# Performance work log

Hardware: AMD Instinct MI355X
Metric: run time of the kernel (lower is better)

## Reference

```python
import jax, jax.numpy as jnp
import numpy as np

M = 262144      # total tokens
K = 64          # n_channels (input dim)
N = 64          # expert_size (output dim)
E = 8           # n_experts


def setup_inputs() -> dict:
    key = jax.random.key(0)
    k1, k2, k3 = jax.random.split(key, 3)
    x = jax.random.normal(k1, (M, K), dtype=jnp.float32)
    sel = jax.random.randint(k2, (M,), 0, E, dtype=jnp.int32)
    w = jax.random.normal(k3, (E, K, N), dtype=jnp.float32)
    return {"x": x, "sel": sel, "w": w}


def reference(x, sel, w):
    # cvmm: out[m] = x[m] @ w[sel[m]]  (per-token expert GEMM)
    # Loop over the small fixed expert set; accumulate masked dense GEMMs
    # instead of materializing w[sel] ([M,K,N], which would be huge).
    E_ = w.shape[0]
    out = jnp.zeros((x.shape[0], w.shape[2]), dtype=x.dtype)
    for e in range(E_):
        mask = (sel == e)[:, None]           # [M,1]
        out = out + jnp.where(mask, x @ w[e], jnp.zeros((), x.dtype))
    return out
```

## Files before the change

kernel.cpp:

```cpp
#include <hip/hip_runtime.h>


typedef __bf16 bf16x8 __attribute__((ext_vector_type(8)));
typedef float floatx4 __attribute__((ext_vector_type(4)));

#define MT 8

__global__ __launch_bounds__(256, 4) void cvmm_kernel(
    const float* __restrict__ x,
    const int* __restrict__ sel,
    const float* __restrict__ w,
    float* __restrict__ out,
    int M)
{
    const int lane = threadIdx.x & 63;
    const int wave = threadIdx.x >> 6;
    const int n0   = wave << 4;
    const int quad = lane >> 4;
    const int l16  = lane & 15;

    floatx4 bfp[8][2];
#pragma unroll
    for (int e = 0; e < 8; ++e) {
#pragma unroll
        for (int t = 0; t < 2; ++t) {
            const float* wp = w + ((e * 64 + t * 32 + quad * 8) * 64) + (n0 + l16);
            bf16x8 f;
#pragma unroll
            for (int j = 0; j < 8; ++j) {
                f[j] = (__bf16)wp[j * 64];
            }
            bfp[e][t] = __builtin_bit_cast(floatx4, f);
        }
    }
#pragma unroll
    for (int e = 0; e < 8; ++e) {
#pragma unroll
        for (int t = 0; t < 2; ++t) {
            asm volatile("" : "+v"(bfp[e][t]));
        }
    }

    bf16x8 zf;
#pragma unroll
    for (int j = 0; j < 8; ++j) zf[j] = (__bf16)0.0f;

    const int mt0 = blockIdx.x * MT;

    floatx4 pa0, pa1, pa2, pa3;
    int ps;
    {
        const int m0 = mt0 << 4;
        const float* xp = x + (size_t)(m0 + l16) * 64 + quad * 8;
        pa0 = *(const floatx4*)(xp);
        pa1 = *(const floatx4*)(xp + 4);
        pa2 = *(const floatx4*)(xp + 32);
        pa3 = *(const floatx4*)(xp + 36);
        ps  = sel[m0 + l16];
    }

#pragma unroll
    for (int i = 0; i < MT; ++i) {
        const floatx4 a0 = pa0, a1 = pa1, a2 = pa2, a3 = pa3;
        const int s = ps;

        if (i + 1 < MT) {
            const int m0n = (mt0 + i + 1) << 4;
            const float* xp = x + (size_t)(m0n + l16) * 64 + quad * 8;
            pa0 = *(const floatx4*)(xp);
            pa1 = *(const floatx4*)(xp + 4);
            pa2 = *(const floatx4*)(xp + 32);
            pa3 = *(const floatx4*)(xp + 36);
            ps  = sel[m0n + l16];
        }

        bf16x8 af0, af1;
#pragma unroll
        for (int j = 0; j < 4; ++j) {
            af0[j]     = (__bf16)a0[j];
            af0[j + 4] = (__bf16)a1[j];
            af1[j]     = (__bf16)a2[j];
            af1[j + 4] = (__bf16)a3[j];
        }

        floatx4 c0 = {0.0f, 0.0f, 0.0f, 0.0f};
        floatx4 c1 = {0.0f, 0.0f, 0.0f, 0.0f};
#pragma unroll
        for (int e = 0; e < 8; ++e) {
            const bool ok = (s == e);
            bf16x8 a0m = ok ? af0 : zf;
            bf16x8 a1m = ok ? af1 : zf;
            c0 = __builtin_amdgcn_mfma_f32_16x16x32_bf16(
                     a0m, __builtin_bit_cast(bf16x8, bfp[e][0]), c0, 0, 0, 0);
            c1 = __builtin_amdgcn_mfma_f32_16x16x32_bf16(
                     a1m, __builtin_bit_cast(bf16x8, bfp[e][1]), c1, 0, 0, 0);
        }

        const int m0 = (mt0 + i) << 4;
        float* op = out + (size_t)(m0 + quad * 4) * 64 + n0 + l16;
#pragma unroll
        for (int r = 0; r < 4; ++r) {
            op[(size_t)r * 64] = c0[r] + c1[r];
        }
    }
}

extern "C" void kernel_launch(void* const* d_in, const int* in_sizes, int n_in,
                              void* d_out, int out_size, void* d_ws, size_t ws_size,
                              hipStream_t stream) {
    const float* x   = (const float*)d_in[0];
    const int*   sel = (const int*)d_in[1];
    const float* w   = (const float*)d_in[2];
    float*       out = (float*)d_out;

    const int M = in_sizes[0] / 64;
    const int mtiles = M / 16;
    const int blocks = (mtiles + MT - 1) / MT;

    cvmm_kernel<<<blocks, 256, 0, stream>>>(x, sel, w, out, M);
}
```

Baseline: 145.7 us.

## Stage x tiles through swizzled double-buffered LDS, converting to bf16 once

Before this change, each of the four waves loaded and converted the full 16x64 x tile itself, so every block read and converted x four times. Now the block cooperatively loads 64-token chunks with coalesced float4 loads and converts them to bf16 once. It writes them into XOR-swizzled, double-buffered LDS that the waves read as MFMA A fragments. The next chunk is prefetched into registers while the current one computes. This costs LDS capacity and a __syncthreads per chunk, and the launch now assumes M is divisible by 256.

```diff
diff --git a/kernel.cpp b/kernel.cpp
--- a/kernel.cpp
+++ b/kernel.cpp
@@ -2,9 +2,11 @@
 
 
 typedef __bf16 bf16x8 __attribute__((ext_vector_type(8)));
-typedef float floatx4 __attribute__((ext_vector_type(4)));
+typedef __bf16 bf16x4 __attribute__((ext_vector_type(4)));
+typedef float  floatx4 __attribute__((ext_vector_type(4)));
 
-#define MT 8
+#define NCHUNK 4
+#define CHUNK_LDS 8192
 
 __global__ __launch_bounds__(256, 4) void cvmm_kernel(
     const float* __restrict__ x,
@@ -13,95 +15,111 @@
     float* __restrict__ out,
     int M)
 {
-    const int lane = threadIdx.x & 63;
-    const int wave = threadIdx.x >> 6;
-    const int n0   = wave << 4;
-    const int quad = lane >> 4;
+    __shared__ __align__(16) unsigned char lds[2 * CHUNK_LDS];
+
+    const int T    = threadIdx.x;
+    const int lane = T & 63;
+    const int wv   = T >> 6;
+    const int q    = lane >> 4;
     const int l16  = lane & 15;
+    const int n0   = wv << 4;
 
     floatx4 bfp[8][2];
 #pragma unroll
     for (int e = 0; e < 8; ++e) {
 #pragma unroll
         for (int t = 0; t < 2; ++t) {
-            const float* wp = w + ((e * 64 + t * 32 + quad * 8) * 64) + (n0 + l16);
+            const float* wp = w + ((e * 64 + t * 32 + q * 8) * 64) + (n0 + l16);
             bf16x8 f;
 #pragma unroll
-            for (int j = 0; j < 8; ++j) {
-                f[j] = (__bf16)wp[j * 64];
-            }
+            for (int j = 0; j < 8; ++j) f[j] = (__bf16)wp[j * 64];
             bfp[e][t] = __builtin_bit_cast(floatx4, f);
         }
     }
 #pragma unroll
-    for (int e = 0; e < 8; ++e) {
+    for (int e = 0; e < 8; ++e)
 #pragma unroll
-        for (int t = 0; t < 2; ++t) {
+        for (int t = 0; t < 2; ++t)
             asm volatile("" : "+v"(bfp[e][t]));
-        }
-    }
 
     bf16x8 zf;
 #pragma unroll
     for (int j = 0; j < 8; ++j) zf[j] = (__bf16)0.0f;
 
-    const int mt0 = blockIdx.x * MT;
+    const int wrow  = T >> 4;
+    const int wbase = wrow * 128 + (((((T & 15) >> 1)) ^ (wrow & 7)) << 4) + (T & 1) * 8;
+    const int roff0 = l16 * 128 + (((q    ) ^ (l16 & 7)) << 4);
+    const int roff1 = l16 * 128 + (((q + 4) ^ (l16 & 7)) << 4);
 
-    floatx4 pa0, pa1, pa2, pa3;
-    int ps;
+    const long tok0 = (long)blockIdx.x * (NCHUNK * 64);
+
+    floatx4 R0, R1, R2, R3;
+    int Sc0, Sc1, Sc2, Sc3, Sn0, Sn1, Sn2, Sn3;
     {
-        const int m0 = mt0 << 4;
-        const float* xp = x + (size_t)(m0 + l16) * 64 + quad * 8;
-        pa0 = *(const floatx4*)(xp);
-        pa1 = *(const floatx4*)(xp + 4);
-        pa2 = *(const floatx4*)(xp + 32);
-        pa3 = *(const floatx4*)(xp + 36);
-        ps  = sel[m0 + l16];
+        const float* xc = x + tok0 * 64;
+        R0 = *(const floatx4*)(xc + 0 * 1024 + 4 * T);
+        R1 = *(const floatx4*)(xc + 1 * 1024 + 4 * T);
+        R2 = *(const floatx4*)(xc + 2 * 1024 + 4 * T);
+        R3 = *(const floatx4*)(xc + 3 * 1024 + 4 * T);
+        const int* sp = sel + tok0 + l16;
+        Sc0 = sp[0]; Sc1 = sp[16]; Sc2 = sp[32]; Sc3 = sp[48];
     }
 
+    int buf = 0;
 #pragma unroll
-    for (int i = 0; i < MT; ++i) {
-        const floatx4 a0 = pa0, a1 = pa1, a2 = pa2, a3 = pa3;
-        const int s = ps;
+    for (int c = 0; c < NCHUNK; ++c) {
+        unsigned char* lb = &lds[buf * CHUNK_LDS];
+#define STAGE(p, Rv)                                                   \
+        {                                                              \
+            bf16x4 v;                                                  \
+            v[0] = (__bf16)Rv[0]; v[1] = (__bf16)Rv[1];                \
+            v[2] = (__bf16)Rv[2]; v[3] = (__bf16)Rv[3];                \
+            *(bf16x4*)(lb + (p) * 2048 + wbase) = v;                   \
+        }
+        STAGE(0, R0) STAGE(1, R1) STAGE(2, R2) STAGE(3, R3)
+#undef STAGE
 
-        if (i + 1 < MT) {
-            const int m0n = (mt0 + i + 1) << 4;
-            const float* xp = x + (size_t)(m0n + l16) * 64 + quad * 8;
-            pa0 = *(const floatx4*)(xp);
-            pa1 = *(const floatx4*)(xp + 4);
-            pa2 = *(const floatx4*)(xp + 32);
-            pa3 = *(const floatx4*)(xp + 36);
-            ps  = sel[m0n + l16];
+        __syncthreads();
+
+        if (c + 1 < NCHUNK) {
+            const float* xc = x + (tok0 + (c + 1) * 64) * 64;
+            R0 = *(const floatx4*)(xc + 0 * 1024 + 4 * T);
+            R1 = *(const floatx4*)(xc + 1 * 1024 + 4 * T);
+            R2 = *(const floatx4*)(xc + 2 * 1024 + 4 * T);
+            R3 = *(const floatx4*)(xc + 3 * 1024 + 4 * T);
+            const int* sp = sel + tok0 + (c + 1) * 64 + l16;
+            Sn0 = sp[0]; Sn1 = sp[16]; Sn2 = sp[32]; Sn3 = sp[48];
         }
 
-        bf16x8 af0, af1;
 #pragma unroll
-        for (int j = 0; j < 4; ++j) {
-            af0[j]     = (__bf16)a0[j];
-            af0[j + 4] = (__bf16)a1[j];
-            af1[j]     = (__bf16)a2[j];
-            af1[j + 4] = (__bf16)a3[j];
+        for (int i = 0; i < 4; ++i) {
+            const bf16x8 af0 = *(const bf16x8*)(lb + i * 2048 + roff0);
+            const bf16x8 af1 = *(const bf16x8*)(lb + i * 2048 + roff1);
+            const int s = (i == 0) ? Sc0 : (i == 1) ? Sc1 : (i == 2) ? Sc2 : Sc3;
+
+            floatx4 c0 = {0.0f, 0.0f, 0.0f, 0.0f};
+            floatx4 c1 = {0.0f, 0.0f, 0.0f, 0.0f};
+#pragma unroll
+            for (int e = 0; e < 8; ++e) {
+                const bool ok = (s == e);
+                bf16x8 a0m = ok ? af0 : zf;
+                bf16x8 a1m = ok ? af1 : zf;
+                c0 = __builtin_amdgcn_mfma_f32_16x16x32_bf16(
+                         a0m, __builtin_bit_cast(bf16x8, bfp[e][0]), c0, 0, 0, 0);
+                c1 = __builtin_amdgcn_mfma_f32_16x16x32_bf16(
+                         a1m, __builtin_bit_cast(bf16x8, bfp[e][1]), c1, 0, 0, 0);
+            }
+
+            const long m0 = tok0 + c * 64 + i * 16;
+            float* op = out + (m0 + q * 4) * 64 + n0 + l16;
+#pragma unroll
+            for (int r = 0; r < 4; ++r) {
+                op[(long)r * 64] = c0[r] + c1[r];
+            }
         }
 
-        floatx4 c0 = {0.0f, 0.0f, 0.0f, 0.0f};
-        floatx4 c1 = {0.0f, 0.0f, 0.0f, 0.0f};
-#pragma unroll
-        for (int e = 0; e < 8; ++e) {
-            const bool ok = (s == e);
-            bf16x8 a0m = ok ? af0 : zf;
-            bf16x8 a1m = ok ? af1 : zf;
-            c0 = __builtin_amdgcn_mfma_f32_16x16x32_bf16(
-                     a0m, __builtin_bit_cast(bf16x8, bfp[e][0]), c0, 0, 0, 0);
-            c1 = __builtin_amdgcn_mfma_f32_16x16x32_bf16(
-                     a1m, __builtin_bit_cast(bf16x8, bfp[e][1]), c1, 0, 0, 0);
-        }
-
-        const int m0 = (mt0 + i) << 4;
-        float* op = out + (size_t)(m0 + quad * 4) * 64 + n0 + l16;
-#pragma unroll
-        for (int r = 0; r < 4; ++r) {
-            op[(size_t)r * 64] = c0[r] + c1[r];
-        }
+        Sc0 = Sn0; Sc1 = Sn1; Sc2 = Sn2; Sc3 = Sn3;
+        buf ^= 1;
     }
 }
 
@@ -114,8 +132,7 @@
     float*       out = (float*)d_out;
 
     const int M = in_sizes[0] / 64;
-    const int mtiles = M / 16;
-    const int blocks = (mtiles + MT - 1) / MT;
+    const int blocks = M / (NCHUNK * 64);
 
     cvmm_kernel<<<blocks, 256, 0, stream>>>(x, sel, w, out, M);
 }
```

Result: faster. 126.1 us (-13.5%).
